# Performance work log

Hardware: AMD Instinct MI355X
Metric: run time of the kernel (lower is better)

## Reference

```python
import jax, jax.numpy as jnp
import numpy as np

RANK_W, SP_W, ANS_W = 1.0, 1.0, 1.0


def _listmle(thres, scores, labels):
    # thres [B,1], scores [B,P], labels [B,P] with values in {-1,0,1}
    fs = jnp.concatenate([thres, scores], axis=1)                      # [B,K]
    fl = jnp.concatenate([jnp.full_like(thres, 0.5), labels], axis=1)  # [B,K]
    s = jnp.exp(fs) * (fl != -1.0).astype(fs.dtype)
    # rest[b,j] = sum_k s[b,k] * (fl[b,k] < fl[b,j])  (sorting in the original
    # is only used to enumerate; with the 0.5 break it reduces to masking
    # entries with label >= 0.5)
    less = (fl[:, None, :] < fl[:, :, None]).astype(fs.dtype)          # [B,j,k]
    rest = jnp.einsum('bjk,bk->bj', less, s)
    mask = fl >= 0.5
    den = jnp.where(mask, s + rest, 1.0)
    logp = jnp.where(mask, fs - jnp.log(den), 0.0)  # log(s_j/(s_j+rest)) with s_j=exp(fs_j)
    return -jnp.sum(logp)


def setup_inputs() -> dict:
    key = jax.random.key(0)
    B, S, H, NS, NP, A = 8, 4096, 1024, 64, 32, 8
    ks = jax.random.split(key, 12)
    sequence_output = jax.random.normal(ks[0], (B, S, H), jnp.float32)
    token_type_ids = jax.random.randint(ks[1], (B, S), 0, 2).astype(jnp.int32)
    # strictly increasing sentence boundaries; last 4 sentences padded with -1
    base = jnp.round(jnp.linspace(8, S - 8, NS + 1)).astype(jnp.int32)
    sent_starts = jnp.broadcast_to(base, (B, NS + 1)).copy()
    sent_starts = sent_starts.at[:, -4:].set(-1)
    para_starts = jnp.sort(jax.random.randint(ks[2], (B, NP), 0, S), axis=1).astype(jnp.int32)
    para_labels = jax.random.randint(ks[3], (B, NP), -1, 2).astype(jnp.float32)
    sp_sent_labels = jax.random.randint(ks[4], (B, NS), -1, 2).astype(jnp.float32)
    starts = jax.random.randint(ks[5], (B, A), -1, S).astype(jnp.int32)
    ends = jax.random.randint(ks[6], (B, A), -1, S).astype(jnp.int32)
    Wqa = jax.random.normal(ks[7], (H, 2), jnp.float32) * 0.02
    bqa = jnp.zeros((2,), jnp.float32)
    Wrank = jax.random.normal(ks[8], (H, 1), jnp.float32) * 0.02
    brank = jnp.zeros((1,), jnp.float32)
    Wsp = jax.random.normal(ks[9], (H, 1), jnp.float32) * 0.02
    bsp = jnp.zeros((1,), jnp.float32)
    return {"sequence_output": sequence_output, "token_type_ids": token_type_ids,
            "sent_starts": sent_starts, "para_starts": para_starts,
            "para_labels": para_labels, "sp_sent_labels": sp_sent_labels,
            "starts": starts, "ends": ends, "Wqa": Wqa, "bqa": bqa,
            "Wrank": Wrank, "brank": brank, "Wsp": Wsp, "bsp": bsp}


def reference(sequence_output, token_type_ids, sent_starts, para_starts,
              para_labels, sp_sent_labels, starts, ends,
              Wqa, bqa, Wrank, brank, Wsp, bsp):
    B, S, H = sequence_output.shape
    logits = sequence_output @ Wqa + bqa                               # [B,S,2]
    tt1 = token_type_ids == 1
    start_logits = jnp.where(tt1, logits[..., 0], -jnp.inf)
    end_logits = jnp.where(tt1, logits[..., 1], -jnp.inf)

    rank_thres = sequence_output[:, 0, :] @ Wrank + brank              # [B,1]
    sent_thres = sequence_output[:, 0, :] @ Wsp + bsp                  # [B,1]

    # ragged per-sentence mean pooling via prefix sums
    csum = jnp.concatenate([jnp.zeros((B, 1, H), sequence_output.dtype),
                            jnp.cumsum(sequence_output, axis=1)], axis=1)  # [B,S+1,H]
    st = sent_starts[:, :-1]
    en = sent_starts[:, 1:]
    valid = en != -1                                                   # [B,NS]
    st_c = jnp.clip(st, 0, S)
    en_c = jnp.maximum(jnp.clip(en, 0, S), st_c + 1)
    NS = st.shape[1]
    g_en = jnp.take_along_axis(csum, jnp.broadcast_to(en_c[:, :, None], (B, NS, H)), axis=1)
    g_st = jnp.take_along_axis(csum, jnp.broadcast_to(st_c[:, :, None], (B, NS, H)), axis=1)
    seg_mean = (g_en - g_st) / (en_c - st_c)[:, :, None].astype(sequence_output.dtype)
    sent_rep = jnp.where(valid[:, :, None], seg_mean, sequence_output[:, -1:, :])
    sp_score = (sent_rep @ Wsp + bsp)[..., 0]                          # [B,NS]

    NP = para_starts.shape[1]
    para_rep = jnp.take_along_axis(
        sequence_output, jnp.broadcast_to(para_starts[:, :, None].astype(jnp.int32), (B, NP, H)), axis=1)
    para_score = (para_rep @ Wrank + brank)[..., 0]                    # [B,NP]

    rank_loss = _listmle(rank_thres, para_score, para_labels)
    sp_loss = _listmle(sent_thres, sp_score, sp_sent_labels)

    ls_start = jax.nn.log_softmax(start_logits, axis=-1)
    ls_end = jax.nn.log_softmax(end_logits, axis=-1)

    def ce(ls, tgt):  # CrossEntropy with ignore_index=-1, reduction='none'
        safe = jnp.clip(tgt, 0, S - 1)
        nll = -jnp.take_along_axis(ls, safe, axis=1)
        return jnp.where(tgt == -1, 0.0, nll)

    loss_tensor = ce(ls_start, starts) + ce(ls_end, ends)              # [B,A]
    lp = -loss_tensor
    lp = jnp.where(lp == 0.0, -jnp.inf, lp)
    m = jnp.sum(jnp.exp(lp), axis=1)                                   # [B]
    pos = m > 0
    span_loss = -jnp.sum(jnp.where(pos, jnp.log(jnp.where(pos, m, 1.0)), 0.0))

    loss = rank_loss * RANK_W + span_loss * ANS_W + sp_loss * SP_W
    return (loss, rank_loss * RANK_W, sp_loss * SP_W)
```

## Files before the change

### kernel.cpp

```cpp
#include <hip/hip_runtime.h>
#include <math.h>

#define B 8
#define S 4096
#define H 1024
#define NSEG 64
#define NPARA 32
#define NA 8
#define BS (B * S)
#define ROWS_PER_BLK 16
#define BLKS_PER_B (S / ROWS_PER_BLK)
#define NBLK (B * BLKS_PER_B)

__device__ __forceinline__ float2 lse_merge(float2 A, float2 Bv)
{
    float m = fmaxf(A.x, Bv.x);
    float s = 0.f;
    if (A.y > 0.f)  s += A.y * expf(A.x - m);
    if (Bv.y > 0.f) s += Bv.y * expf(Bv.x - m);
    return make_float2(m, s);
}

__global__ __launch_bounds__(256) void dots_kernel(
    const float* __restrict__ seq,
    const float* __restrict__ Wqa,
    const float* __restrict__ Wsp,
    const float* __restrict__ Wrank,
    const int*   __restrict__ tt,
    float* __restrict__ scores,
    float4* __restrict__ lse_part,
    float* __restrict__ out)
{
    if (blockIdx.x == 0 && threadIdx.x == 0) {
        out[0] = 0.f; out[1] = 0.f; out[2] = 0.f;
    }
    const int blk   = blockIdx.x;
    const int b     = blk >> 8;
    const int rbase = (blk & 255) * ROWS_PER_BLK;
    const int w     = threadIdx.x >> 6;
    const int lane  = threadIdx.x & 63;

    __shared__ float  blkres[4][ROWS_PER_BLK];
    __shared__ float4 lsep[4];

    float wq0[4][4], wq1[4][4];
    float4 wspv[4], wrkv[4];
#pragma unroll
    for (int c = 0; c < 4; ++c) {
        int h0 = (lane + 64 * c) * 4;
#pragma unroll
        for (int j = 0; j < 4; ++j) {
            wq0[c][j] = Wqa[(h0 + j) * 2 + 0];
            wq1[c][j] = Wqa[(h0 + j) * 2 + 1];
        }
        wspv[c] = *(const float4*)(Wsp + h0);
        wrkv[c] = *(const float4*)(Wrank + h0);
    }

    const int* ttb = tt + b * S;
    float m0 = -INFINITY, s0 = 0.f, m1 = -INFINITY, s1 = 0.f;

    for (int i = 0; i < 4; ++i) {
        const int srow = rbase + w * 4 + i;
        const float4* row = (const float4*)(seq + ((size_t)b * S + srow) * H);
        float a0 = 0.f, a1 = 0.f, a2 = 0.f, a3 = 0.f;
#pragma unroll
        for (int c = 0; c < 4; ++c) {
            float4 v = row[lane + 64 * c];
            a0 += v.x * wq0[c][0] + v.y * wq0[c][1] + v.z * wq0[c][2] + v.w * wq0[c][3];
            a1 += v.x * wq1[c][0] + v.y * wq1[c][1] + v.z * wq1[c][2] + v.w * wq1[c][3];
            a2 += v.x * wspv[c].x + v.y * wspv[c].y + v.z * wspv[c].z + v.w * wspv[c].w;
            a3 += v.x * wrkv[c].x + v.y * wrkv[c].y + v.z * wrkv[c].z + v.w * wrkv[c].w;
        }
#pragma unroll
        for (int off = 32; off > 0; off >>= 1) {
            a0 += __shfl_xor(a0, off);
            a1 += __shfl_xor(a1, off);
            a2 += __shfl_xor(a2, off);
            a3 += __shfl_xor(a3, off);
        }
        if (ttb[srow] == 1) {
            float mn = fmaxf(m0, a0);
            s0 = s0 * expf(m0 - mn) + expf(a0 - mn); m0 = mn;
            mn = fmaxf(m1, a1);
            s1 = s1 * expf(m1 - mn) + expf(a1 - mn); m1 = mn;
        }
        if (lane == 0) {
            const int idx = w * 4 + i;
            blkres[0][idx] = a0; blkres[1][idx] = a1;
            blkres[2][idx] = a2; blkres[3][idx] = a3;
        }
    }
    if (lane == 0) lsep[w] = make_float4(m0, s0, m1, s1);
    __syncthreads();

    const int t = threadIdx.x;
    if (t < 64) {
        const int p = t >> 4, idx = t & 15;
        scores[p * BS + b * S + rbase + idx] = blkres[p][idx];
    }
    if (t == 0) {
        float2 L0 = make_float2(lsep[0].x, lsep[0].y);
        float2 L1 = make_float2(lsep[0].z, lsep[0].w);
#pragma unroll
        for (int i = 1; i < 4; ++i) {
            L0 = lse_merge(L0, make_float2(lsep[i].x, lsep[i].y));
            L1 = lse_merge(L1, make_float2(lsep[i].z, lsep[i].w));
        }
        lse_part[blk] = make_float4(L0.x, L0.y, L1.x, L1.y);
    }
}

__device__ __forceinline__ float blk_reduce1(float v, float* wred1, int t)
{
    const int lane = t & 63, w = t >> 6;
#pragma unroll
    for (int off = 32; off > 0; off >>= 1) v += __shfl_xor(v, off);
    if (lane == 0) wred1[w] = v;
    __syncthreads();
    float r = wred1[0] + wred1[1] + wred1[2] + wred1[3];
    __syncthreads();
    return r;
}

__device__ float listmle_block(const float* fs, const float* fl, float* se,
                               int n, float* wred1, int t)
{
    if (t < n) se[t] = (fl[t] != -1.0f) ? expf(fs[t]) : 0.0f;
    __syncthreads();
    float lp = 0.0f;
    if (t < n && fl[t] >= 0.5f) {
        float fj = fl[t];
        float rest = 0.0f;
        for (int k = 0; k < n; ++k)
            if (fl[k] < fj) rest += se[k];
        lp = fs[t] - logf(se[t] + rest);
    }
    float tot = blk_reduce1(lp, wred1, t);
    return -tot;
}

__global__ __launch_bounds__(256) void batch_kernel(
    const float*  __restrict__ scores,
    const float4* __restrict__ lse_part,
    const int*    __restrict__ tt,
    const int*    __restrict__ sent_starts,
    const int*    __restrict__ para_starts,
    const float*  __restrict__ para_labels,
    const float*  __restrict__ sp_labels,
    const int*    __restrict__ starts,
    const int*    __restrict__ ends,
    float* __restrict__ out)
{
    const int b = blockIdx.x;
    const int t = threadIdx.x;
    const int lane = t & 63, w = t >> 6;

    __shared__ float4 lsew[4];
    __shared__ float  wred1[4];
    __shared__ float  fsb[1 + NSEG], flb[1 + NSEG], seb[1 + NSEG];
    __shared__ float  lse_sh[2];
    __shared__ int    ssh[NSEG + 1];

    const float* p0 = scores + 0 * BS + b * S;
    const float* p1 = scores + 1 * BS + b * S;
    const float* p2 = scores + 2 * BS + b * S;
    const float* p3 = scores + 3 * BS + b * S;
    const int*   ttb = tt + b * S;

    if (t < NSEG + 1) ssh[t] = sent_starts[b * (NSEG + 1) + t];

    {
        float4 P = lse_part[b * BLKS_PER_B + t];
        float2 L0 = make_float2(P.x, P.y);
        float2 L1 = make_float2(P.z, P.w);
#pragma unroll
        for (int off = 32; off > 0; off >>= 1) {
            float2 O0 = make_float2(__shfl_xor(L0.x, off), __shfl_xor(L0.y, off));
            float2 O1 = make_float2(__shfl_xor(L1.x, off), __shfl_xor(L1.y, off));
            L0 = lse_merge(L0, O0);
            L1 = lse_merge(L1, O1);
        }
        if (lane == 0) lsew[w] = make_float4(L0.x, L0.y, L1.x, L1.y);
        __syncthreads();
        if (t == 0) {
            float2 M0 = make_float2(lsew[0].x, lsew[0].y);
            float2 M1 = make_float2(lsew[0].z, lsew[0].w);
#pragma unroll
            for (int i = 1; i < 4; ++i) {
                M0 = lse_merge(M0, make_float2(lsew[i].x, lsew[i].y));
                M1 = lse_merge(M1, make_float2(lsew[i].z, lsew[i].w));
            }
            lse_sh[0] = M0.x + logf(M0.y);
            lse_sh[1] = M1.x + logf(M1.y);
        }
    }

    {
        const int j  = t >> 2;
        const int l4 = t & 3;
        int st = ssh[j];
        int en = ssh[j + 1];
        if (en != -1) {
            int stc = min(max(st, 0), S);
            int enc = max(min(max(en, 0), S), stc + 1);
            float x = 0.f;
            for (int s = stc + l4; s < enc; s += 4) x += p2[s];
            x += __shfl_xor(x, 1);
            x += __shfl_xor(x, 2);
            if (l4 == 0) {
                fsb[1 + j] = x / (float)(enc - stc);
                flb[1 + j] = sp_labels[b * NSEG + j];
            }
        } else {
            if (l4 == 0) {
                fsb[1 + j] = p2[S - 1];
                flb[1 + j] = sp_labels[b * NSEG + j];
            }
        }
        if (t == 0) { fsb[0] = p2[0]; flb[0] = 0.5f; }
    }
    __syncthreads();
    float sp_loss_b = listmle_block(fsb, flb, seb, 1 + NSEG, wred1, t);

    if (t == 0) { fsb[0] = p3[0]; flb[0] = 0.5f; }
    if (t < NPARA) {
        int ps = para_starts[b * NPARA + t];
        fsb[1 + t] = p3[ps];
        flb[1 + t] = para_labels[b * NPARA + t];
    }
    __syncthreads();
    float rank_loss_b = listmle_block(fsb, flb, seb, 1 + NPARA, wred1, t);

    float e_a = 0.f;
    if (t < NA) {
        const float lse0 = lse_sh[0], lse1 = lse_sh[1];
        int tsv = starts[b * NA + t];
        int tev = ends[b * NA + t];
        float lt = 0.f;
        if (tsv != -1) {
            int sf = min(max(tsv, 0), S - 1);
            float sl = (ttb[sf] == 1) ? p0[sf] : -INFINITY;
            lt += -(sl - lse0);
        }
        if (tev != -1) {
            int sf = min(max(tev, 0), S - 1);
            float el = (ttb[sf] == 1) ? p1[sf] : -INFINITY;
            lt += -(el - lse1);
        }
        float lp = -lt;
        e_a = (lp == 0.0f) ? 0.f : expf(lp);
    }
#pragma unroll
    for (int off = 4; off > 0; off >>= 1) e_a += __shfl_xor(e_a, off, 8);
    if (t == 0) {
        float logm = (e_a > 0.f) ? logf(e_a) : 0.f;
        atomicAdd(out + 0, rank_loss_b + sp_loss_b - logm);
        atomicAdd(out + 1, rank_loss_b);
        atomicAdd(out + 2, sp_loss_b);
    }
}

extern "C" void kernel_launch(void* const* d_in, const int* in_sizes, int n_in,
                              void* d_out, int out_size, void* d_ws, size_t ws_size,
                              hipStream_t stream)
{
    const float* seq         = (const float*)d_in[0];
    const int*   tt          = (const int*)  d_in[1];
    const int*   sent_starts = (const int*)  d_in[2];
    const int*   para_starts = (const int*)  d_in[3];
    const float* para_labels = (const float*)d_in[4];
    const float* sp_labels   = (const float*)d_in[5];
    const int*   starts      = (const int*)  d_in[6];
    const int*   ends        = (const int*)  d_in[7];
    const float* Wqa         = (const float*)d_in[8];
    const float* Wrank       = (const float*)d_in[10];
    const float* Wsp         = (const float*)d_in[12];

    float*  out      = (float*)d_out;
    float*  scores   = (float*)d_ws;
    float4* lse_part = (float4*)(scores + 4 * (size_t)BS);

    dots_kernel<<<NBLK, 256, 0, stream>>>(seq, Wqa, Wsp, Wrank, tt,
                                          scores, lse_part, out);
    batch_kernel<<<B, 256, 0, stream>>>(scores, lse_part, tt, sent_starts,
                                        para_starts, para_labels, sp_labels,
                                        starts, ends, out);
}
```

Before: 38.51 us.

## Fuse sentence segment sums into dots kernel and vectorize Wqa loads

The dots kernel now maps each of its 16 rows to a sentence segment and accumulates per-block partial sums of the sp score, assuming at most two segments per block (jlo and the next one). The batch kernel then merges these partials with shared-memory atomics instead of re-reading roughly 4096 p2 scores per batch in a serial-ish loop. Wqa weights are loaded as float4 pairs instead of scalar strided loads. This adds extra syncs and a segment lookup in the hot kernel, and it gives wrong sums if a 16-row block spans more than two segments or if a segment boundary is skipped.

```diff
diff --git a/kernel.cpp b/kernel.cpp
--- a/kernel.cpp
+++ b/kernel.cpp
@@ -22,13 +22,15 @@
 }
 
 __global__ __launch_bounds__(256) void dots_kernel(
-    const float* __restrict__ seq,
-    const float* __restrict__ Wqa,
-    const float* __restrict__ Wsp,
-    const float* __restrict__ Wrank,
-    const int*   __restrict__ tt,
+    const float4* __restrict__ seq4,
+    const float4* __restrict__ Wqa4,
+    const float4* __restrict__ Wsp4,
+    const float4* __restrict__ Wrank4,
+    const int*    __restrict__ tt,
+    const int*    __restrict__ sent_starts,
     float* __restrict__ scores,
     float4* __restrict__ lse_part,
+    float4* __restrict__ segpart,
     float* __restrict__ out)
 {
     if (blockIdx.x == 0 && threadIdx.x == 0) {
@@ -39,36 +41,60 @@
     const int rbase = (blk & 255) * ROWS_PER_BLK;
     const int w     = threadIdx.x >> 6;
     const int lane  = threadIdx.x & 63;
+    const int t     = threadIdx.x;
 
     __shared__ float  blkres[4][ROWS_PER_BLK];
     __shared__ float4 lsep[4];
-
-    float wq0[4][4], wq1[4][4];
-    float4 wspv[4], wrkv[4];
+    __shared__ float2 wacc[4];
+    __shared__ int    ssh[NSEG + 1];
+    __shared__ int    rowseg[ROWS_PER_BLK];
+    __shared__ int    jlo_sh;
+
+    float4 qA[4], qB[4], wspv[4], wrkv[4];
 #pragma unroll
     for (int c = 0; c < 4; ++c) {
-        int h0 = (lane + 64 * c) * 4;
-#pragma unroll
-        for (int j = 0; j < 4; ++j) {
-            wq0[c][j] = Wqa[(h0 + j) * 2 + 0];
-            wq1[c][j] = Wqa[(h0 + j) * 2 + 1];
-        }
-        wspv[c] = *(const float4*)(Wsp + h0);
-        wrkv[c] = *(const float4*)(Wrank + h0);
-    }
+        const int ch = lane + 64 * c;
+        qA[c]   = Wqa4[2 * ch];
+        qB[c]   = Wqa4[2 * ch + 1];
+        wspv[c] = Wsp4[ch];
+        wrkv[c] = Wrank4[ch];
+    }
+
+    if (t < NSEG + 1) ssh[t] = sent_starts[b * (NSEG + 1) + t];
+    __syncthreads();
+    if (t < ROWS_PER_BLK) {
+        const int r = rbase + t;
+        int j = -1;
+        for (int k = 0; k < NSEG; ++k) {
+            int en = ssh[k + 1];
+            if (en == -1) break;
+            if (r >= ssh[k] && r < en) { j = k; break; }
+        }
+        rowseg[t] = j;
+    }
+    __syncthreads();
+    if (t == 0) {
+        int jl = -1;
+        for (int i = 0; i < ROWS_PER_BLK; ++i)
+            if (rowseg[i] >= 0) { jl = rowseg[i]; break; }
+        jlo_sh = jl;
+    }
+    __syncthreads();
+    const int jlo = jlo_sh;
 
     const int* ttb = tt + b * S;
     float m0 = -INFINITY, s0 = 0.f, m1 = -INFINITY, s1 = 0.f;
+    float segA = 0.f, segB = 0.f;
 
     for (int i = 0; i < 4; ++i) {
         const int srow = rbase + w * 4 + i;
-        const float4* row = (const float4*)(seq + ((size_t)b * S + srow) * H);
+        const float4* row = seq4 + ((size_t)b * S + srow) * (H / 4);
         float a0 = 0.f, a1 = 0.f, a2 = 0.f, a3 = 0.f;
 #pragma unroll
         for (int c = 0; c < 4; ++c) {
             float4 v = row[lane + 64 * c];
-            a0 += v.x * wq0[c][0] + v.y * wq0[c][1] + v.z * wq0[c][2] + v.w * wq0[c][3];
-            a1 += v.x * wq1[c][0] + v.y * wq1[c][1] + v.z * wq1[c][2] + v.w * wq1[c][3];
+            a0 += v.x * qA[c].x   + v.y * qA[c].z   + v.z * qB[c].x   + v.w * qB[c].z;
+            a1 += v.x * qA[c].y   + v.y * qA[c].w   + v.z * qB[c].y   + v.w * qB[c].w;
             a2 += v.x * wspv[c].x + v.y * wspv[c].y + v.z * wspv[c].z + v.w * wspv[c].w;
             a3 += v.x * wrkv[c].x + v.y * wrkv[c].y + v.z * wrkv[c].z + v.w * wrkv[c].w;
         }
@@ -85,16 +111,17 @@
             mn = fmaxf(m1, a1);
             s1 = s1 * expf(m1 - mn) + expf(a1 - mn); m1 = mn;
         }
+        const int j = rowseg[w * 4 + i];
+        if (j >= 0) { if (j == jlo) segA += a2; else segB += a2; }
         if (lane == 0) {
             const int idx = w * 4 + i;
             blkres[0][idx] = a0; blkres[1][idx] = a1;
             blkres[2][idx] = a2; blkres[3][idx] = a3;
         }
     }
-    if (lane == 0) lsep[w] = make_float4(m0, s0, m1, s1);
-    __syncthreads();
-
-    const int t = threadIdx.x;
+    if (lane == 0) { lsep[w] = make_float4(m0, s0, m1, s1); wacc[w] = make_float2(segA, segB); }
+    __syncthreads();
+
     if (t < 64) {
         const int p = t >> 4, idx = t & 15;
         scores[p * BS + b * S + rbase + idx] = blkres[p][idx];
@@ -102,12 +129,15 @@
     if (t == 0) {
         float2 L0 = make_float2(lsep[0].x, lsep[0].y);
         float2 L1 = make_float2(lsep[0].z, lsep[0].w);
+        float SA = wacc[0].x, SB = wacc[0].y;
 #pragma unroll
         for (int i = 1; i < 4; ++i) {
             L0 = lse_merge(L0, make_float2(lsep[i].x, lsep[i].y));
             L1 = lse_merge(L1, make_float2(lsep[i].z, lsep[i].w));
+            SA += wacc[i].x; SB += wacc[i].y;
         }
         lse_part[blk] = make_float4(L0.x, L0.y, L1.x, L1.y);
+        segpart[blk]  = make_float4(__int_as_float(jlo), SA, SB, 0.f);
     }
 }
 
@@ -143,6 +173,7 @@
 __global__ __launch_bounds__(256) void batch_kernel(
     const float*  __restrict__ scores,
     const float4* __restrict__ lse_part,
+    const float4* __restrict__ segpart,
     const int*    __restrict__ tt,
     const int*    __restrict__ sent_starts,
     const int*    __restrict__ para_starts,
@@ -157,10 +188,11 @@
     const int lane = t & 63, w = t >> 6;
 
     __shared__ float4 lsew[4];
+    __shared__ float  segsum[NSEG + 2];
+    __shared__ int    ssh[NSEG + 1];
     __shared__ float  wred1[4];
     __shared__ float  fsb[1 + NSEG], flb[1 + NSEG], seb[1 + NSEG];
     __shared__ float  lse_sh[2];
-    __shared__ int    ssh[NSEG + 1];
 
     const float* p0 = scores + 0 * BS + b * S;
     const float* p1 = scores + 1 * BS + b * S;
@@ -168,7 +200,9 @@
     const float* p3 = scores + 3 * BS + b * S;
     const int*   ttb = tt + b * S;
 
+    if (t < NSEG + 2) segsum[t] = 0.f;
     if (t < NSEG + 1) ssh[t] = sent_starts[b * (NSEG + 1) + t];
+    __syncthreads();
 
     {
         float4 P = lse_part[b * BLKS_PER_B + t];
@@ -182,43 +216,41 @@
             L1 = lse_merge(L1, O1);
         }
         if (lane == 0) lsew[w] = make_float4(L0.x, L0.y, L1.x, L1.y);
-        __syncthreads();
-        if (t == 0) {
-            float2 M0 = make_float2(lsew[0].x, lsew[0].y);
-            float2 M1 = make_float2(lsew[0].z, lsew[0].w);
-#pragma unroll
-            for (int i = 1; i < 4; ++i) {
-                M0 = lse_merge(M0, make_float2(lsew[i].x, lsew[i].y));
-                M1 = lse_merge(M1, make_float2(lsew[i].z, lsew[i].w));
-            }
-            lse_sh[0] = M0.x + logf(M0.y);
-            lse_sh[1] = M1.x + logf(M1.y);
-        }
-    }
-
-    {
-        const int j  = t >> 2;
-        const int l4 = t & 3;
-        int st = ssh[j];
-        int en = ssh[j + 1];
+
+        float4 SP = segpart[b * BLKS_PER_B + t];
+        int jl = __float_as_int(SP.x);
+        if (jl >= 0) {
+            atomicAdd(&segsum[jl], SP.y);
+            atomicAdd(&segsum[jl + 1], SP.z);
+        }
+    }
+    __syncthreads();
+    if (t == 0) {
+        float2 M0 = make_float2(lsew[0].x, lsew[0].y);
+        float2 M1 = make_float2(lsew[0].z, lsew[0].w);
+#pragma unroll
+        for (int i = 1; i < 4; ++i) {
+            M0 = lse_merge(M0, make_float2(lsew[i].x, lsew[i].y));
+            M1 = lse_merge(M1, make_float2(lsew[i].z, lsew[i].w));
+        }
+        lse_sh[0] = M0.x + logf(M0.y);
+        lse_sh[1] = M1.x + logf(M1.y);
+    }
+
+    if (t == 0) { fsb[0] = p2[0]; flb[0] = 0.5f; }
+    if (t < NSEG) {
+        int st = ssh[t];
+        int en = ssh[t + 1];
+        float score;
         if (en != -1) {
             int stc = min(max(st, 0), S);
             int enc = max(min(max(en, 0), S), stc + 1);
-            float x = 0.f;
-            for (int s = stc + l4; s < enc; s += 4) x += p2[s];
-            x += __shfl_xor(x, 1);
-            x += __shfl_xor(x, 2);
-            if (l4 == 0) {
-                fsb[1 + j] = x / (float)(enc - stc);
-                flb[1 + j] = sp_labels[b * NSEG + j];
-            }
+            score = segsum[t] / (float)(enc - stc);
         } else {
-            if (l4 == 0) {
-                fsb[1 + j] = p2[S - 1];
-                flb[1 + j] = sp_labels[b * NSEG + j];
-            }
-        }
-        if (t == 0) { fsb[0] = p2[0]; flb[0] = 0.5f; }
+            score = p2[S - 1];
+        }
+        fsb[1 + t] = score;
+        flb[1 + t] = sp_labels[b * NSEG + t];
     }
     __syncthreads();
     float sp_loss_b = listmle_block(fsb, flb, seb, 1 + NSEG, wred1, t);
@@ -280,10 +312,15 @@
     float*  out      = (float*)d_out;
     float*  scores   = (float*)d_ws;
     float4* lse_part = (float4*)(scores + 4 * (size_t)BS);
-
-    dots_kernel<<<NBLK, 256, 0, stream>>>(seq, Wqa, Wsp, Wrank, tt,
-                                          scores, lse_part, out);
-    batch_kernel<<<B, 256, 0, stream>>>(scores, lse_part, tt, sent_starts,
-                                        para_starts, para_labels, sp_labels,
-                                        starts, ends, out);
-}
+    float4* segpart  = lse_part + NBLK;
+
+    dots_kernel<<<NBLK, 256, 0, stream>>>((const float4*)seq,
+                                          (const float4*)Wqa,
+                                          (const float4*)Wsp,
+                                          (const float4*)Wrank,
+                                          tt, sent_starts,
+                                          scores, lse_part, segpart, out);
+    batch_kernel<<<B, 256, 0, stream>>>(scores, lse_part, segpart, tt,
+                                        sent_starts, para_starts, para_labels,
+                                        sp_labels, starts, ends, out);
+}
```

Result: slower. 43.75 us (+13.6%).
